# Performance work log

Hardware: AMD Instinct MI355X
Metric: run time of the kernel (lower is better)

## Reference

```python
import jax, jax.numpy as jnp
import numpy as np

D_MODEL = 1024
N_HEADS = 16
D_FF = 4096
HEAD_DIM = D_MODEL // N_HEADS
EPS = 1e-5


def setup_inputs() -> dict:
    key = jax.random.key(0)
    ks = jax.random.split(key, 12)
    B, S, D = 2, 2048, D_MODEL
    s = 0.02
    return {
        "x": jax.random.normal(ks[0], (B, S, D), jnp.float32),
        "ln1_g": jnp.ones((D,), jnp.float32),
        "ln1_b": jnp.zeros((D,), jnp.float32),
        "qkv_w": jax.random.normal(ks[1], (3 * D, D), jnp.float32) * s,
        "qkv_b": jnp.zeros((3 * D,), jnp.float32),
        "out_w": jax.random.normal(ks[2], (D, D), jnp.float32) * s,
        "out_b": jnp.zeros((D,), jnp.float32),
        "ln2_g": jnp.ones((D,), jnp.float32),
        "ln2_b": jnp.zeros((D,), jnp.float32),
        "fc1_w": jax.random.normal(ks[3], (D_FF, D), jnp.float32) * s,
        "fc1_b": jnp.zeros((D_FF,), jnp.float32),
        "fc2_w": jax.random.normal(ks[4], (D, D_FF), jnp.float32) * s,
        "fc2_b": jnp.zeros((D,), jnp.float32),
    }


def _layernorm(x, g, b):
    mu = jnp.mean(x, axis=-1, keepdims=True)
    var = jnp.mean(jnp.square(x - mu), axis=-1, keepdims=True)
    return (x - mu) * jax.lax.rsqrt(var + EPS) * g + b


def _attention(h, qkv_w, qkv_b, out_w, out_b):
    B, S, D = h.shape
    qkv = h @ qkv_w.T + qkv_b  # [B,S,3D]
    q, k, v = jnp.split(qkv, 3, axis=-1)
    # [B,H,S,hd]
    q = q.reshape(B, S, N_HEADS, HEAD_DIM).transpose(0, 2, 1, 3)
    k = k.reshape(B, S, N_HEADS, HEAD_DIM).transpose(0, 2, 1, 3)
    v = v.reshape(B, S, N_HEADS, HEAD_DIM).transpose(0, 2, 1, 3)
    scale = HEAD_DIM ** -0.5
    scores = jnp.einsum("bhqd,bhkd->bhqk", q, k) * scale
    causal = jnp.tril(jnp.ones((S, S), bool))
    scores = jnp.where(causal, scores, -jnp.inf)
    attn = jax.nn.softmax(scores, axis=-1)
    out = jnp.einsum("bhqk,bhkd->bhqd", attn, v)
    out = out.transpose(0, 2, 1, 3).reshape(B, S, D)
    return out @ out_w.T + out_b


def reference(x, ln1_g, ln1_b, qkv_w, qkv_b, out_w, out_b,
              ln2_g, ln2_b, fc1_w, fc1_b, fc2_w, fc2_b):
    x = x + _attention(_layernorm(x, ln1_g, ln1_b), qkv_w, qkv_b, out_w, out_b)
    h = _layernorm(x, ln2_g, ln2_b)
    ff = jax.nn.gelu(h @ fc1_w.T + fc1_b, approximate=False) @ fc2_w.T + fc2_b
    return x + ff
```

## Files before the change

### kernel.cpp

```cpp
#include <hip/hip_runtime.h>
#include <stdint.h>

typedef uint16_t u16;
typedef uint32_t u32;
typedef __bf16 bf16_t;
typedef bf16_t bf16x8 __attribute__((ext_vector_type(8)));
typedef float f32x4 __attribute__((ext_vector_type(4)));
typedef u16 u16x4 __attribute__((ext_vector_type(4)));
typedef u16 u16x8 __attribute__((ext_vector_type(8)));

__device__ __forceinline__ float bf2f(u16 v) {
    union { u32 u; float f; } x; x.u = ((u32)v) << 16; return x.f;
}
__device__ __forceinline__ u16 f2bf(float f) {
    union { float f; u32 u; } x; x.f = f;
    u32 r = (x.u + 0x7fffu + ((x.u >> 16) & 1u)) >> 16;
    return (u16)r;
}

__device__ __forceinline__ void gload_lds16(const u16* g, u16* l) {
    __builtin_amdgcn_global_load_lds(
        (const __attribute__((address_space(1))) void*)g,
        (__attribute__((address_space(3))) void*)l,
        16, 0, 0);
}
#define WAITVM(n) __builtin_amdgcn_s_waitcnt(0x0F70 | (n))
#define WAIT_LGKM0() __builtin_amdgcn_s_waitcnt(0xC07F)
#define BARRIER() __builtin_amdgcn_s_barrier()

__global__ __launch_bounds__(256) void cvt4_kernel(
    const float* __restrict__ s0, const float* __restrict__ s1,
    const float* __restrict__ s2, const float* __restrict__ s3,
    u16* __restrict__ d0, u16* __restrict__ d1,
    u16* __restrict__ d2, u16* __restrict__ d3)
{
    int i = blockIdx.x * 256 + threadIdx.x;
    const float* s; u16* d; int off;
    if (i < 786432)       { s = s0; d = d0; off = i; }
    else if (i < 1048576) { s = s1; d = d1; off = i - 786432; }
    else if (i < 2097152) { s = s2; d = d2; off = i - 1048576; }
    else                  { s = s3; d = d3; off = i - 2097152; }
    f32x4 v = ((const f32x4*)s)[off];
    u16x4 o;
#pragma unroll
    for (int j = 0; j < 4; j++) o[j] = f2bf(v[j]);
    ((u16x4*)d)[off] = o;
}

__global__ __launch_bounds__(256) void ln_kernel(
    const float* __restrict__ x, const float* __restrict__ g,
    const float* __restrict__ b, u16* __restrict__ out)
{
    const int row = blockIdx.x;
    const int tid = threadIdx.x;
    f32x4 xv = *(const f32x4*)(x + (size_t)row * 1024 + tid * 4);
    float v[4];
    float s = 0.f, s2 = 0.f;
#pragma unroll
    for (int i = 0; i < 4; i++) { v[i] = xv[i]; s += v[i]; s2 += v[i] * v[i]; }
#pragma unroll
    for (int off = 1; off < 64; off <<= 1) {
        s  += __shfl_xor(s, off);
        s2 += __shfl_xor(s2, off);
    }
    __shared__ float ws1[4], ws2[4];
    if ((tid & 63) == 0) { ws1[tid >> 6] = s; ws2[tid >> 6] = s2; }
    __syncthreads();
    s  = ws1[0] + ws1[1] + ws1[2] + ws1[3];
    s2 = ws2[0] + ws2[1] + ws2[2] + ws2[3];
    float mu  = s * (1.0f / 1024.0f);
    float var = s2 * (1.0f / 1024.0f) - mu * mu;
    float rstd = rsqrtf(var + 1e-5f);
    f32x4 gv = *(const f32x4*)(g + tid * 4);
    f32x4 bv = *(const f32x4*)(b + tid * 4);
    u16x4 ov;
#pragma unroll
    for (int i = 0; i < 4; i++)
        ov[i] = f2bf((v[i] - mu) * rstd * gv[i] + bv[i]);
    *(u16x4*)(out + (size_t)row * 1024 + tid * 4) = ov;
}

__global__ __launch_bounds__(256, 2) void gemm_bt(
    const u16* __restrict__ A, const u16* __restrict__ Bt,
    const float* __restrict__ bias, const float* res,
    void* C, int N, int K, int lda, int gelu)
{
    __shared__ __align__(16) u16 sA[2][128 * 32];
    __shared__ __align__(16) u16 sB[2][128 * 32];
    const int tid  = threadIdx.x;
    const int wave = tid >> 6, lane = tid & 63;
    const int lm = lane & 15, quad = lane >> 4;
    const int wm = wave >> 1, wn = wave & 1;
    const int row0 = blockIdx.y * 128, col0 = blockIdx.x * 128;
    const int r16 = lane >> 2;
    const int c8  = (lane & 3) * 8;
    const int niter = K >> 5;

    const u16* gsrc;
    size_t gstride;
    int chunk0;
    if (wave < 2) {
        chunk0 = wave * 4;
        gsrc = A + (size_t)(row0 + chunk0 * 16 + r16) * lda + c8;
        gstride = lda;
    } else {
        chunk0 = (wave - 2) * 4;
        gsrc = Bt + (size_t)(col0 + chunk0 * 16 + r16) * K + c8;
        gstride = K;
    }
    u16* lbase0 = (wave < 2) ? &sA[0][chunk0 * 512] : &sB[0][chunk0 * 512];
    u16* lbase1 = (wave < 2) ? &sA[1][chunk0 * 512] : &sB[1][chunk0 * 512];

    f32x4 acc[4][4];
#pragma unroll
    for (int i = 0; i < 4; i++)
#pragma unroll
        for (int j = 0; j < 4; j++) acc[i][j] = f32x4{0.f, 0.f, 0.f, 0.f};

#pragma unroll
    for (int j = 0; j < 4; j++)
        gload_lds16(gsrc + (size_t)(j * 16) * gstride, lbase0 + j * 512);

    for (int k = 0; k < niter; k++) {
        const int cur = k & 1;
        if (k + 1 < niter) {
            const u16* gs = gsrc + (size_t)(k + 1) * 32;
            u16* lb = cur ? lbase0 : lbase1;
#pragma unroll
            for (int j = 0; j < 4; j++)
                gload_lds16(gs + (size_t)(j * 16) * gstride, lb + j * 512);
            WAITVM(4);
        } else {
            WAITVM(0);
        }
        BARRIER();

        bf16x8 af[4], bfr[4];
#pragma unroll
        for (int t = 0; t < 4; t++)
            af[t] = *(const bf16x8*)&sA[cur][(wm * 64 + t * 16 + lm) * 32 + quad * 8];
#pragma unroll
        for (int t = 0; t < 4; t++)
            bfr[t] = *(const bf16x8*)&sB[cur][(wn * 64 + t * 16 + lm) * 32 + quad * 8];
#pragma unroll
        for (int i = 0; i < 4; i++)
#pragma unroll
            for (int j = 0; j < 4; j++)
                acc[i][j] = __builtin_amdgcn_mfma_f32_16x16x32_bf16(af[i], bfr[j], acc[i][j], 0, 0, 0);

        BARRIER();
    }

    float bj[4];
#pragma unroll
    for (int j = 0; j < 4; j++) bj[j] = bias[col0 + wn * 64 + j * 16 + lm];
#pragma unroll
    for (int i = 0; i < 4; i++) {
        int rbase = row0 + wm * 64 + i * 16 + quad * 4;
#pragma unroll
        for (int j = 0; j < 4; j++) {
            int c = col0 + wn * 64 + j * 16 + lm;
#pragma unroll
            for (int r = 0; r < 4; r++) {
                float v = acc[i][j][r] + bj[j];
                if (gelu) v = 0.5f * v * (1.0f + erff(v * 0.70710678118f));
                size_t idx = (size_t)(rbase + r) * N + c;
                if (res) {
                    ((float*)C)[idx] = v + res[idx];
                } else {
                    ((u16*)C)[idx] = f2bf(v);
                }
            }
        }
    }
}

__global__ __launch_bounds__(256, 2) void gemm_bt64(
    const u16* __restrict__ A, const u16* __restrict__ Bt,
    const float* __restrict__ bias, const float* res,
    void* C, int N, int K, int lda, int gelu)
{
    __shared__ __align__(16) u16 sA[2][128 * 32];
    __shared__ __align__(16) u16 sB[2][64 * 32];
    const int tid  = threadIdx.x;
    const int wave = tid >> 6, lane = tid & 63;
    const int lm = lane & 15, quad = lane >> 4;
    const int wm = wave >> 1, wn = wave & 1;
    const int row0 = blockIdx.y * 128, col0 = blockIdx.x * 64;
    const int r16 = lane >> 2;
    const int c8  = (lane & 3) * 8;
    const int niter = K >> 5;

    const u16* gs_[3];
    u16* lb0_[3];
    u16* lb1_[3];
#pragma unroll
    for (int j = 0; j < 3; j++) {
        int cid = wave * 3 + j;
        if (cid < 8) {
            gs_[j] = A + (size_t)(row0 + cid * 16 + r16) * lda + c8;
            lb0_[j] = &sA[0][cid * 512];
            lb1_[j] = &sA[1][cid * 512];
        } else {
            int bc = cid - 8;
            gs_[j] = Bt + (size_t)(col0 + bc * 16 + r16) * K + c8;
            lb0_[j] = &sB[0][bc * 512];
            lb1_[j] = &sB[1][bc * 512];
        }
    }

    f32x4 acc[4][2];
#pragma unroll
    for (int i = 0; i < 4; i++)
#pragma unroll
        for (int j = 0; j < 2; j++) acc[i][j] = f32x4{0.f, 0.f, 0.f, 0.f};

#pragma unroll
    for (int j = 0; j < 3; j++) gload_lds16(gs_[j], lb0_[j]);

    for (int k = 0; k < niter; k++) {
        const int cur = k & 1;
        if (k + 1 < niter) {
#pragma unroll
            for (int j = 0; j < 3; j++)
                gload_lds16(gs_[j] + (size_t)(k + 1) * 32, cur ? lb0_[j] : lb1_[j]);
            WAITVM(3);
        } else {
            WAITVM(0);
        }
        BARRIER();

        bf16x8 af[4], bfr[2];
#pragma unroll
        for (int t = 0; t < 4; t++)
            af[t] = *(const bf16x8*)&sA[cur][(wm * 64 + t * 16 + lm) * 32 + quad * 8];
#pragma unroll
        for (int t = 0; t < 2; t++)
            bfr[t] = *(const bf16x8*)&sB[cur][(wn * 32 + t * 16 + lm) * 32 + quad * 8];
#pragma unroll
        for (int i = 0; i < 4; i++)
#pragma unroll
            for (int j = 0; j < 2; j++)
                acc[i][j] = __builtin_amdgcn_mfma_f32_16x16x32_bf16(af[i], bfr[j], acc[i][j], 0, 0, 0);

        BARRIER();
    }

    float bj[2];
#pragma unroll
    for (int j = 0; j < 2; j++) bj[j] = bias[col0 + wn * 32 + j * 16 + lm];
#pragma unroll
    for (int i = 0; i < 4; i++) {
        int rbase = row0 + wm * 64 + i * 16 + quad * 4;
#pragma unroll
        for (int j = 0; j < 2; j++) {
            int c = col0 + wn * 32 + j * 16 + lm;
#pragma unroll
            for (int r = 0; r < 4; r++) {
                float v = acc[i][j][r] + bj[j];
                if (gelu) v = 0.5f * v * (1.0f + erff(v * 0.70710678118f));
                size_t idx = (size_t)(rbase + r) * N + c;
                if (res) {
                    ((float*)C)[idx] = v + res[idx];
                } else {
                    ((u16*)C)[idx] = f2bf(v);
                }
            }
        }
    }
}

__global__ __launch_bounds__(256, 4) void attn_kernel(u16* qkv)
{
    __shared__ __align__(16) u16 sQP[64 * 64];
    __shared__ __align__(16) u16 sK[2][64 * 64];
    __shared__ __align__(16) u16 sVT[2][64 * 64];

    const int tid  = threadIdx.x;
    const int wave = tid >> 6, lane = tid & 63;
    const int lm = lane & 15, quad = lane >> 4;
    int xi = blockIdx.x;
    int qz = (xi & 1) ? (31 - (xi >> 1)) : (xi >> 1);
    int qi = ((blockIdx.y >> 3) & 1) ? (31 - qz) : qz;
    const int q0 = qi * 64;
    const int b = blockIdx.y >> 4, h = blockIdx.y & 15;
    const size_t tok0 = (size_t)b * 2048;
    const int qcol = h * 64, kcol = 1024 + h * 64, vcol = 2048 + h * 64;
    const int r8 = lane >> 3;
    const int c8s = (((lane & 7) ^ r8) << 3);

    const int vkey = tid >> 2;
    const int vq   = tid & 3;
    const int vdq  = vq * 16;
    const u16* vbase = qkv + (tok0 + vkey) * 3072 + vcol + vdq;

#pragma unroll
    for (int j = 0; j < 2; j++) {
        int chunk = wave * 2 + j;
        int r = chunk * 8 + r8;
        gload_lds16(qkv + (tok0 + q0 + r) * 3072 + qcol + c8s, &sQP[chunk * 512]);
    }
#pragma unroll
    for (int j = 0; j < 2; j++) {
        int chunk = wave * 2 + j;
        int r = chunk * 8 + r8;
        gload_lds16(qkv + (tok0 + r) * 3072 + kcol + c8s, &sK[0][chunk * 512]);
    }
    u16x8 va = *(const u16x8*)vbase;
    u16x8 vb = *(const u16x8*)(vbase + 8);
    WAITVM(4);
    BARRIER();

    bf16x8 aq[2];
#pragma unroll
    for (int kk = 0; kk < 2; kk++)
        aq[kk] = *(const bf16x8*)
            &sQP[(wave * 16 + lm) * 64 + (((kk * 4 + quad) ^ (lm & 7)) << 3)];

    f32x4 oacc[4];
    float mrun = -1e30f, lrun = 0.f;
#pragma unroll
    for (int n = 0; n < 4; n++) oacc[n] = f32x4{0.f, 0.f, 0.f, 0.f};

    u16* sPw = &sQP[wave * 16 * 64];
    const int ntiles = qi + 1;
    const int qrow_lane = q0 + wave * 16 + lm;

    for (int tk = 0; tk < ntiles; tk++) {
        const int cur = tk & 1;
        u16x8 na = va, nb = vb;
        if (tk + 1 < ntiles) {
            const int kb1 = (tk + 1) * 64;
#pragma unroll
            for (int j = 0; j < 2; j++) {
                int chunk = wave * 2 + j;
                int r = chunk * 8 + r8;
                gload_lds16(qkv + (tok0 + kb1 + r) * 3072 + kcol + c8s,
                            &sK[1 - cur][chunk * 512]);
            }
            const u16* vr = vbase + (size_t)kb1 * 3072;
            na = *(const u16x8*)vr;
            nb = *(const u16x8*)(vr + 8);
            WAITVM(4);
        } else {
            WAITVM(0);
        }
#pragma unroll
        for (int i = 0; i < 8; i++) {
            int d = vdq + i;
            sVT[cur][d * 64 + ((((vkey >> 3) ^ i ^ vq)) << 3) + (vkey & 7)] = va[i];
        }
#pragma unroll
        for (int i = 0; i < 8; i++) {
            int d = vdq + 8 + i;
            sVT[cur][d * 64 + ((((vkey >> 3) ^ i ^ vq)) << 3) + (vkey & 7)] = vb[i];
        }
        va = na; vb = nb;
        WAIT_LGKM0();
        BARRIER();

        const int kb = tk * 64;
        float sc[4][4];
#pragma unroll
        for (int n = 0; n < 4; n++) {
            f32x4 s = f32x4{0.f, 0.f, 0.f, 0.f};
#pragma unroll
            for (int kk = 0; kk < 2; kk++) {
                bf16x8 ak = *(const bf16x8*)
                    &sK[cur][(n * 16 + lm) * 64 + (((kk * 4 + quad) ^ (lm & 7)) << 3)];
                s = __builtin_amdgcn_mfma_f32_16x16x32_bf16(ak, aq[kk], s, 0, 0, 0);
            }
#pragma unroll
            for (int r = 0; r < 4; r++) {
                int key = kb + n * 16 + quad * 4 + r;
                sc[n][r] = (key <= qrow_lane) ? s[r] * 0.125f : -1e30f;
            }
        }
        float mx = sc[0][0];
#pragma unroll
        for (int n = 0; n < 4; n++)
#pragma unroll
            for (int r = 0; r < 4; r++) mx = fmaxf(mx, sc[n][r]);
        mx = fmaxf(mx, __shfl_xor(mx, 16));
        mx = fmaxf(mx, __shfl_xor(mx, 32));
        float mnew  = fmaxf(mrun, mx);
        float alpha = __expf(mrun - mnew);
        float sum = 0.f;
#pragma unroll
        for (int n = 0; n < 4; n++)
#pragma unroll
            for (int r = 0; r < 4; r++) {
                float p = __expf(sc[n][r] - mnew);
                sc[n][r] = p;
                sum += p;
            }
        sum += __shfl_xor(sum, 16);
        sum += __shfl_xor(sum, 32);
        lrun = lrun * alpha + sum;
        mrun = mnew;
        float aT[4];
#pragma unroll
        for (int r = 0; r < 4; r++) aT[r] = __shfl(alpha, quad * 4 + r);
#pragma unroll
        for (int n = 0; n < 4; n++)
#pragma unroll
            for (int r = 0; r < 4; r++) oacc[n][r] *= aT[r];
#pragma unroll
        for (int n = 0; n < 4; n++)
#pragma unroll
            for (int r = 0; r < 4; r++) {
                int key = n * 16 + quad * 4 + r;
                int addr = lm * 64 + (((key >> 3) ^ (lm & 7)) << 3) + (key & 7);
                sPw[addr] = f2bf(sc[n][r]);
            }
        bf16x8 ap[2];
#pragma unroll
        for (int kk = 0; kk < 2; kk++)
            ap[kk] = *(const bf16x8*)
                &sPw[lm * 64 + (((kk * 4 + quad) ^ (lm & 7)) << 3)];
#pragma unroll
        for (int n = 0; n < 4; n++)
#pragma unroll
            for (int kk = 0; kk < 2; kk++) {
                bf16x8 bv = *(const bf16x8*)
                    &sVT[cur][(n * 16 + lm) * 64 +
                              ((((kk * 4 + quad) ^ (lm & 7) ^ n)) << 3)];
                oacc[n] = __builtin_amdgcn_mfma_f32_16x16x32_bf16(ap[kk], bv, oacc[n], 0, 0, 0);
            }

        BARRIER();
    }

    {
        float lT[4];
#pragma unroll
        for (int r = 0; r < 4; r++) lT[r] = __shfl(lrun, quad * 4 + r);
        int rowb = q0 + wave * 16 + quad * 4;
#pragma unroll
        for (int r = 0; r < 4; r++) {
            float inv = 1.0f / lT[r];
#pragma unroll
            for (int n = 0; n < 4; n++) {
                int d = n * 16 + lm;
                qkv[(tok0 + rowb + r) * 3072 + qcol + d] = f2bf(oacc[n][r] * inv);
            }
        }
    }
}

extern "C" void kernel_launch(void* const* d_in, const int* in_sizes, int n_in,
                              void* d_out, int out_size, void* d_ws, size_t ws_size,
                              hipStream_t stream)
{
    (void)in_sizes; (void)n_in; (void)out_size; (void)ws_size;
    const float* x    = (const float*)d_in[0];
    const float* ln1g = (const float*)d_in[1];
    const float* ln1b = (const float*)d_in[2];
    const float* qkvwF= (const float*)d_in[3];
    const float* qkvb = (const float*)d_in[4];
    const float* outwF= (const float*)d_in[5];
    const float* outb = (const float*)d_in[6];
    const float* ln2g = (const float*)d_in[7];
    const float* ln2b = (const float*)d_in[8];
    const float* fc1wF= (const float*)d_in[9];
    const float* fc1b = (const float*)d_in[10];
    const float* fc2wF= (const float*)d_in[11];
    const float* fc2b = (const float*)d_in[12];
    float* out = (float*)d_out;
    u16*   ws  = (u16*)d_ws;
    const int M1 = 1 << 20;

    u16* qkvw = ws;
    u16* outw = ws + 3 * M1;
    u16* qkvB = ws + 4 * M1;
    u16* ff1  = ws;
    u16* fc1w = ws + 16 * M1;
    u16* fc2w = ws + 20 * M1;
    u16* h    = ws + 24 * M1;

    cvt4_kernel<<<12288, 256, 0, stream>>>(qkvwF, outwF, fc1wF, fc2wF,
                                           qkvw, outw, fc1w, fc2w);

    ln_kernel<<<4096, 256, 0, stream>>>(x, ln1g, ln1b, h);
    gemm_bt<<<dim3(24, 32), 256, 0, stream>>>(h, qkvw, qkvb, nullptr, qkvB,
                                              3072, 1024, 1024, 0);
    attn_kernel<<<dim3(32, 32), 256, 0, stream>>>(qkvB);
    gemm_bt64<<<dim3(16, 32), 256, 0, stream>>>(qkvB, outw, outb, x, out,
                                                1024, 1024, 3072, 0);
    ln_kernel<<<4096, 256, 0, stream>>>(out, ln2g, ln2b, h);
    gemm_bt<<<dim3(32, 32), 256, 0, stream>>>(h, fc1w, fc1b, nullptr, ff1,
                                              4096, 1024, 1024, 1);
    gemm_bt64<<<dim3(16, 32), 256, 0, stream>>>(ff1, fc2w, fc2b, out, out,
                                                1024, 4096, 4096, 0);
}
```

Measured before the change: 368.0 us.

## Triple-buffer GEMM LDS loads, XOR-swizzle LDS layout, and remap blocks across XCDs

Both GEMM kernels go from double to triple LDS buffering, prefetching two K-steps ahead to hide global load latency. The LDS column chunks are XOR-swizzled on both write and read to cut bank conflicts. Block indices are also remapped so neighbouring tiles land on the same XCD, which should improve L2 reuse. The extra buffer raises LDS use to 48KB per block, which may lower occupancy. The remap hardcodes assumptions about grid shape (8 XCDs, by up to 32, gx even), so it could be wrong for other grid sizes.

```diff
diff --git a/kernel.cpp b/kernel.cpp
--- a/kernel.cpp
+++ b/kernel.cpp
@@ -27,6 +27,13 @@
 #define WAITVM(n) __builtin_amdgcn_s_waitcnt(0x0F70 | (n))
 #define WAIT_LGKM0() __builtin_amdgcn_s_waitcnt(0xC07F)
 #define BARRIER() __builtin_amdgcn_s_barrier()
+
+__device__ __forceinline__ void xcd_remap(int gx, int& bx, int& by) {
+    int n = by * gx + bx;
+    int k = n & 7, m = n >> 3;
+    by = ((k & 3) << 3) | (m & 7);
+    bx = (k >> 2) * (gx >> 1) + (m >> 3);
+}
 
 __global__ __launch_bounds__(256) void cvt4_kernel(
     const float* __restrict__ s0, const float* __restrict__ s1,
@@ -85,15 +92,17 @@
     const float* __restrict__ bias, const float* res,
     void* C, int N, int K, int lda, int gelu)
 {
-    __shared__ __align__(16) u16 sA[2][128 * 32];
-    __shared__ __align__(16) u16 sB[2][128 * 32];
+    __shared__ __align__(16) u16 sA[3][128 * 32];
+    __shared__ __align__(16) u16 sB[3][128 * 32];
     const int tid  = threadIdx.x;
     const int wave = tid >> 6, lane = tid & 63;
     const int lm = lane & 15, quad = lane >> 4;
     const int wm = wave >> 1, wn = wave & 1;
-    const int row0 = blockIdx.y * 128, col0 = blockIdx.x * 128;
+    int bx = blockIdx.x, by = blockIdx.y;
+    xcd_remap(gridDim.x, bx, by);
+    const int row0 = by * 128, col0 = bx * 128;
     const int r16 = lane >> 2;
-    const int c8  = (lane & 3) * 8;
+    const int c8x = (((lane & 3) ^ (r16 & 3)) << 3);
     const int niter = K >> 5;
 
     const u16* gsrc;
@@ -101,15 +110,17 @@
     int chunk0;
     if (wave < 2) {
         chunk0 = wave * 4;
-        gsrc = A + (size_t)(row0 + chunk0 * 16 + r16) * lda + c8;
+        gsrc = A + (size_t)(row0 + chunk0 * 16 + r16) * lda + c8x;
         gstride = lda;
     } else {
         chunk0 = (wave - 2) * 4;
-        gsrc = Bt + (size_t)(col0 + chunk0 * 16 + r16) * K + c8;
+        gsrc = Bt + (size_t)(col0 + chunk0 * 16 + r16) * K + c8x;
         gstride = K;
     }
-    u16* lbase0 = (wave < 2) ? &sA[0][chunk0 * 512] : &sB[0][chunk0 * 512];
-    u16* lbase1 = (wave < 2) ? &sA[1][chunk0 * 512] : &sB[1][chunk0 * 512];
+    u16* lb[3];
+#pragma unroll
+    for (int s = 0; s < 3; s++)
+        lb[s] = (wave < 2) ? &sA[s][chunk0 * 512] : &sB[s][chunk0 * 512];
 
     f32x4 acc[4][4];
 #pragma unroll
@@ -119,16 +130,21 @@
 
 #pragma unroll
     for (int j = 0; j < 4; j++)
-        gload_lds16(gsrc + (size_t)(j * 16) * gstride, lbase0 + j * 512);
-
+        gload_lds16(gsrc + (size_t)(j * 16) * gstride, lb[0] + j * 512);
+#pragma unroll
+    for (int j = 0; j < 4; j++)
+        gload_lds16(gsrc + 32 + (size_t)(j * 16) * gstride, lb[1] + j * 512);
+
+    int cur = 0, nxt = 2;
     for (int k = 0; k < niter; k++) {
-        const int cur = k & 1;
-        if (k + 1 < niter) {
-            const u16* gs = gsrc + (size_t)(k + 1) * 32;
-            u16* lb = cur ? lbase0 : lbase1;
+        if (k + 2 < niter) {
+            const u16* gs = gsrc + (size_t)(k + 2) * 32;
+            u16* l = lb[nxt];
 #pragma unroll
             for (int j = 0; j < 4; j++)
-                gload_lds16(gs + (size_t)(j * 16) * gstride, lb + j * 512);
+                gload_lds16(gs + (size_t)(j * 16) * gstride, l + j * 512);
+            WAITVM(8);
+        } else if (k + 1 < niter) {
             WAITVM(4);
         } else {
             WAITVM(0);
@@ -138,10 +154,12 @@
         bf16x8 af[4], bfr[4];
 #pragma unroll
         for (int t = 0; t < 4; t++)
-            af[t] = *(const bf16x8*)&sA[cur][(wm * 64 + t * 16 + lm) * 32 + quad * 8];
+            af[t] = *(const bf16x8*)
+                &sA[cur][(wm * 64 + t * 16 + lm) * 32 + ((quad ^ (lm & 3)) << 3)];
 #pragma unroll
         for (int t = 0; t < 4; t++)
-            bfr[t] = *(const bf16x8*)&sB[cur][(wn * 64 + t * 16 + lm) * 32 + quad * 8];
+            bfr[t] = *(const bf16x8*)
+                &sB[cur][(wn * 64 + t * 16 + lm) * 32 + ((quad ^ (lm & 3)) << 3)];
 #pragma unroll
         for (int i = 0; i < 4; i++)
 #pragma unroll
@@ -149,6 +167,8 @@
                 acc[i][j] = __builtin_amdgcn_mfma_f32_16x16x32_bf16(af[i], bfr[j], acc[i][j], 0, 0, 0);
 
         BARRIER();
+        cur = (cur == 2) ? 0 : cur + 1;
+        nxt = (nxt == 2) ? 0 : nxt + 1;
     }
 
     float bj[4];
@@ -180,32 +200,33 @@
     const float* __restrict__ bias, const float* res,
     void* C, int N, int K, int lda, int gelu)
 {
-    __shared__ __align__(16) u16 sA[2][128 * 32];
-    __shared__ __align__(16) u16 sB[2][64 * 32];
+    __shared__ __align__(16) u16 sA[3][128 * 32];
+    __shared__ __align__(16) u16 sB[3][64 * 32];
     const int tid  = threadIdx.x;
     const int wave = tid >> 6, lane = tid & 63;
     const int lm = lane & 15, quad = lane >> 4;
     const int wm = wave >> 1, wn = wave & 1;
-    const int row0 = blockIdx.y * 128, col0 = blockIdx.x * 64;
+    int bx = blockIdx.x, by = blockIdx.y;
+    xcd_remap(gridDim.x, bx, by);
+    const int row0 = by * 128, col0 = bx * 64;
     const int r16 = lane >> 2;
-    const int c8  = (lane & 3) * 8;
+    const int c8x = (((lane & 3) ^ (r16 & 3)) << 3);
     const int niter = K >> 5;
 
     const u16* gs_[3];
-    u16* lb0_[3];
-    u16* lb1_[3];
+    u16* lb_[3][3];
 #pragma unroll
     for (int j = 0; j < 3; j++) {
         int cid = wave * 3 + j;
         if (cid < 8) {
-            gs_[j] = A + (size_t)(row0 + cid * 16 + r16) * lda + c8;
-            lb0_[j] = &sA[0][cid * 512];
-            lb1_[j] = &sA[1][cid * 512];
+            gs_[j] = A + (size_t)(row0 + cid * 16 + r16) * lda + c8x;
+#pragma unroll
+            for (int s = 0; s < 3; s++) lb_[j][s] = &sA[s][cid * 512];
         } else {
             int bc = cid - 8;
-            gs_[j] = Bt + (size_t)(col0 + bc * 16 + r16) * K + c8;
-            lb0_[j] = &sB[0][bc * 512];
-            lb1_[j] = &sB[1][bc * 512];
+            gs_[j] = Bt + (size_t)(col0 + bc * 16 + r16) * K + c8x;
+#pragma unroll
+            for (int s = 0; s < 3; s++) lb_[j][s] = &sB[s][bc * 512];
         }
     }
 
@@ -216,14 +237,18 @@
         for (int j = 0; j < 2; j++) acc[i][j] = f32x4{0.f, 0.f, 0.f, 0.f};
 
 #pragma unroll
-    for (int j = 0; j < 3; j++) gload_lds16(gs_[j], lb0_[j]);
-
+    for (int j = 0; j < 3; j++) gload_lds16(gs_[j], lb_[j][0]);
+#pragma unroll
+    for (int j = 0; j < 3; j++) gload_lds16(gs_[j] + 32, lb_[j][1]);
+
+    int cur = 0, nxt = 2;
     for (int k = 0; k < niter; k++) {
-        const int cur = k & 1;
-        if (k + 1 < niter) {
+        if (k + 2 < niter) {
 #pragma unroll
             for (int j = 0; j < 3; j++)
-                gload_lds16(gs_[j] + (size_t)(k + 1) * 32, cur ? lb0_[j] : lb1_[j]);
+                gload_lds16(gs_[j] + (size_t)(k + 2) * 32, lb_[j][nxt]);
+            WAITVM(6);
+        } else if (k + 1 < niter) {
             WAITVM(3);
         } else {
             WAITVM(0);
@@ -233,10 +258,12 @@
         bf16x8 af[4], bfr[2];
 #pragma unroll
         for (int t = 0; t < 4; t++)
-            af[t] = *(const bf16x8*)&sA[cur][(wm * 64 + t * 16 + lm) * 32 + quad * 8];
+            af[t] = *(const bf16x8*)
+                &sA[cur][(wm * 64 + t * 16 + lm) * 32 + ((quad ^ (lm & 3)) << 3)];
 #pragma unroll
         for (int t = 0; t < 2; t++)
-            bfr[t] = *(const bf16x8*)&sB[cur][(wn * 32 + t * 16 + lm) * 32 + quad * 8];
+            bfr[t] = *(const bf16x8*)
+                &sB[cur][(wn * 32 + t * 16 + lm) * 32 + ((quad ^ (lm & 3)) << 3)];
 #pragma unroll
         for (int i = 0; i < 4; i++)
 #pragma unroll
@@ -244,6 +271,8 @@
                 acc[i][j] = __builtin_amdgcn_mfma_f32_16x16x32_bf16(af[i], bfr[j], acc[i][j], 0, 0, 0);
 
         BARRIER();
+        cur = (cur == 2) ? 0 : cur + 1;
+        nxt = (nxt == 2) ? 0 : nxt + 1;
     }
 
     float bj[2];
```

After: 370.3 us. About the same (+0.6%).
